# Kernel optimization log

Measured on AMD Instinct MI355X. Metric: run time of the kernel, lower is better.

## Reference

```python
import jax, jax.numpy as jnp
import numpy as np

R = 8
TOP_K_A = 2
TOP_K_B = 2
SCALING = 16.0 / R  # lora_alpha / r


def setup_inputs() -> dict:
    key = jax.random.key(0)
    k1, k2, k3, k4, k5 = jax.random.split(key, 5)
    B, S, D_IN, D_OUT, EA, EB = 4, 2048, 4096, 4096, 8, 8
    x = jax.random.normal(k1, (B, S, D_IN), dtype=jnp.float32)
    router_logits_a = jax.random.normal(k2, (B * S, EA), dtype=jnp.float32)
    router_logits_b = jax.random.normal(k3, (B * S, EB), dtype=jnp.float32)
    # nn.Linear(in, r).weight -> [r, in]; stacked per expert: [E_a, r, in]
    Wa = jax.random.normal(k4, (EA, R, D_IN), dtype=jnp.float32) * (1.0 / np.sqrt(D_IN))
    # nn.Linear(r, out).weight -> [out, r]; stacked: [E_b, out, r]
    Wb = jax.random.normal(k5, (EB, D_OUT, R), dtype=jnp.float32) * (1.0 / np.sqrt(R))
    return {"x": x, "router_logits_a": router_logits_a,
            "router_logits_b": router_logits_b, "Wa": Wa, "Wb": Wb}


def reference(x, router_logits_a, router_logits_b, Wa, Wb):
    B, S, D_IN = x.shape
    flat_x = x.reshape(-1, D_IN)  # [T, D_in]

    # --- A experts: dense compute over all experts, then top-k gather ---
    topk_logits_a, topk_idx_a = jax.lax.top_k(router_logits_a, TOP_K_A)
    weights_a = jax.nn.softmax(topk_logits_a, axis=-1)  # [T, k_a]
    a_all = jnp.einsum('ti,eri->ter', flat_x, Wa)  # [T, E_a, r]
    sel_a = jnp.take_along_axis(a_all, topk_idx_a[:, :, None], axis=1)  # [T, k_a, r]
    mid = jnp.sum(sel_a * weights_a[:, :, None], axis=1)  # [T, r]

    # --- B experts: dense compute over all experts, then top-k gather ---
    b_all = jnp.einsum('tr,eor->teo', mid, Wb)  # [T, E_b, D_out]
    topk_logits_b, topk_idx_b = jax.lax.top_k(router_logits_b, TOP_K_B)
    weights_b = jax.nn.softmax(topk_logits_b, axis=-1)  # [T, k_b]
    sel_b = jnp.take_along_axis(b_all, topk_idx_b[:, :, None], axis=1)  # [T, k_b, D_out]
    out_flat = jnp.sum(sel_b * weights_b[:, :, None], axis=1) * SCALING  # [T, D_out]
    output = out_flat.reshape(B, S, -1)

    # --- load-balancing aux losses (torch.var is unbiased) ---
    probs_a = jnp.mean(jax.nn.softmax(router_logits_a, axis=-1), axis=0)
    probs_b = jnp.mean(jax.nn.softmax(router_logits_b, axis=-1), axis=0)
    aux_loss_a = Wa.shape[0] * jnp.var(probs_a, ddof=1)
    aux_loss_b = Wb.shape[0] * jnp.var(probs_b, ddof=1)
    return output, aux_loss_a, aux_loss_b
```

## Files before the change

kernel.cpp:

```cpp
#include <hip/hip_runtime.h>

#define T_TOK 8192
#define D_IN  4096
#define D_OUT 4096

typedef _Float16 h2 __attribute__((ext_vector_type(2)));
typedef _Float16 h4 __attribute__((ext_vector_type(4)));
typedef _Float16 h8 __attribute__((ext_vector_type(8)));
typedef float    f4v __attribute__((ext_vector_type(4)));

__device__ __forceinline__ h2 pkrtz(float a, float b) {
    auto r = __builtin_amdgcn_cvt_pkrtz(a, b);
    h2 o; __builtin_memcpy(&o, &r, 4); return o;
}
__device__ __forceinline__ h8 cvt8(float4 f0, float4 f1) {
    h2 p0 = pkrtz(f0.x, f0.y), p1 = pkrtz(f0.z, f0.w);
    h2 p2 = pkrtz(f1.x, f1.y), p3 = pkrtz(f1.z, f1.w);
    return (h8){p0.x, p0.y, p1.x, p1.y, p2.x, p2.y, p3.x, p3.y};
}

__device__ __forceinline__ void gl_lds16(const void* g, void* l) {
    __builtin_amdgcn_global_load_lds(
        (const __attribute__((address_space(1))) unsigned int*)g,
        (__attribute__((address_space(3))) unsigned int*)l, 16, 0, 0);
}


__global__ __launch_bounds__(256)
void prep(const float* __restrict__ Wa, const float* __restrict__ Wb,
          const float* __restrict__ la, const float* __restrict__ lb,
          _Float16* __restrict__ WaB, _Float16* __restrict__ WbB,
          double* __restrict__ pax) {
    const int bid = blockIdx.x, tx = threadIdx.x;
    __shared__ double red[4][16];
    if (bid < 256) {
        int gid = bid * 256 + tx;
        int er = gid >> 10, k0 = (gid & 1023) * 4;
        float4 v = ((const float4*)Wa)[gid];
        h2 p0 = pkrtz(v.x, v.y), p1 = pkrtz(v.z, v.w);
        h4 o = { p0.x, p0.y, p1.x, p1.y };
        *(h4*)(WaB + ((k0 >> 3) * 64 + er) * 8 + (k0 & 7)) = o;
    } else if (bid < 384) {
        int gid = (bid - 256) * 256 + tx;
        int e = gid >> 12, o = gid & 4095;
        const float4* p = (const float4*)(Wb + ((size_t)e * 4096 + o) * 8);
        h8 v = cvt8(p[0], p[1]);
        *(h8*)(WbB + ((size_t)e * 4096 + o) * 8) = v;
    } else {
        const int ab = bid - 384;
        const int t = ab * 256 + tx;
        double loc[16];
        {
            float l[8];
#pragma unroll
            for (int i = 0; i < 8; ++i) l[i] = la[(size_t)t * 8 + i];
            float m = l[0];
#pragma unroll
            for (int i = 1; i < 8; ++i) m = fmaxf(m, l[i]);
            float s = 0.f, e[8];
#pragma unroll
            for (int i = 0; i < 8; ++i) { e[i] = __expf(l[i] - m); s += e[i]; }
#pragma unroll
            for (int i = 0; i < 8; ++i) loc[i] = (double)(e[i] / s);
        }
        {
            float l[8];
#pragma unroll
            for (int i = 0; i < 8; ++i) l[i] = lb[(size_t)t * 8 + i];
            float m = l[0];
#pragma unroll
            for (int i = 1; i < 8; ++i) m = fmaxf(m, l[i]);
            float s = 0.f, e[8];
#pragma unroll
            for (int i = 0; i < 8; ++i) { e[i] = __expf(l[i] - m); s += e[i]; }
#pragma unroll
            for (int i = 0; i < 8; ++i) loc[8 + i] = (double)(e[i] / s);
        }
        const int lane = tx & 63, wid = tx >> 6;
#pragma unroll
        for (int v = 0; v < 16; ++v) {
            double s = loc[v];
#pragma unroll
            for (int off = 32; off > 0; off >>= 1) s += __shfl_down(s, off, 64);
            if (lane == 0) red[wid][v] = s;
        }
        __syncthreads();
        if (tx < 16)
            pax[ab * 16 + tx] = red[0][tx] + red[1][tx] + red[2][tx] + red[3][tx];
    }
}

__global__ __launch_bounds__(256)
void fused(const float* __restrict__ x, const _Float16* __restrict__ WaB,
           const _Float16* __restrict__ WbB, const float* __restrict__ la,
           const float* __restrict__ lb, float* __restrict__ out,
           const double* __restrict__ pax) {
    __shared__ union {
        struct { float xb[2][2048]; _Float16 wab[2][8192]; } p1;
        struct { _Float16 wbb[2][8192]; } p3;
    } U;
    __shared__ float    pL[16][66];
    __shared__ _Float16 MbL[1024];
    __shared__ float    sW0[16], sW1[16], sCb[16][8];
    __shared__ int      sE0[16], sE1[16];
    __shared__ double   sl[16];

    const int tx = threadIdx.x, l = tx & 63, w = tx >> 6;
    const int mr = l & 15, kf = l >> 4;
    const int m0 = blockIdx.x * 16;
    const int er1 = w * 16 + mr;

    f4v acc = (f4v){0.f, 0.f, 0.f, 0.f};

#define STAGE1(IT, BUF) do {                                                   \
    _Pragma("unroll") for (int i_ = 0; i_ < 2; ++i_) {                         \
        int j_ = w * 2 + i_;                                                   \
        int row_ = j_ * 2 + (l >> 5);                                          \
        int cb_ = ((l & 31) * 16) ^ ((row_ & 7) << 4);                         \
        const char* src_ = (const char*)x                                      \
            + (((size_t)(m0 + row_) * D_IN + (size_t)(IT) * 128) << 2) + cb_;  \
        gl_lds16(src_, (char*)U.p1.xb[BUF] + j_ * 1024);                       \
    }                                                                          \
    _Pragma("unroll") for (int i_ = 0; i_ < 4; ++i_) {                         \
        int j_ = w * 4 + i_;                                                   \
        const char* src_ = (const char*)WaB + (size_t)(IT) * 16384             \
            + j_ * 1024 + l * 16;                                              \
        gl_lds16(src_, (char*)U.p1.wab[BUF] + j_ * 1024);                      \
    }                                                                          \
  } while (0)

#define CMP1(BUF) do {                                                         \
    const char* xb_ = (const char*)U.p1.xb[BUF] + mr * 512;                    \
    const int sw_ = (mr & 7) << 4;                                             \
    _Pragma("unroll") for (int ks_ = 0; ks_ < 4; ++ks_) {                      \
        int c0_ = ks_ * 128 + kf * 32;                                         \
        float4 f0_ = *(const float4*)(xb_ + ((c0_) ^ sw_));                    \
        float4 f1_ = *(const float4*)(xb_ + ((c0_ + 16) ^ sw_));               \
        h8 a_ = cvt8(f0_, f1_);                                                \
        h8 b_ = *(const h8*)((const char*)U.p1.wab[BUF]                        \
                             + ((ks_ * 4 + kf) * 64 + er1) * 16);              \
        acc = __builtin_amdgcn_mfma_f32_16x16x32_f16(a_, b_, acc, 0, 0, 0);    \
    }                                                                          \
  } while (0)

    STAGE1(0, 0);
    __syncthreads();
#pragma unroll 1
    for (int it = 0; it < 32; ++it) {
        if (it < 31) STAGE1(it + 1, (it & 1) ^ 1);
        CMP1(it & 1);
        __syncthreads();
    }
#undef STAGE1
#undef CMP1

#pragma unroll
    for (int r = 0; r < 4; ++r) pL[kf * 4 + r][er1] = acc[r];
    __syncthreads();

    if (tx < 16) {
        const int t = tx;
        float lg[8];
#pragma unroll
        for (int i = 0; i < 8; ++i) lg[i] = la[(size_t)(m0 + t) * 8 + i];
        int e0 = 0; float b0 = lg[0];
#pragma unroll
        for (int i = 1; i < 8; ++i) if (lg[i] > b0) { b0 = lg[i]; e0 = i; }
        int e1 = -1; float b1 = -1e30f;
#pragma unroll
        for (int i = 0; i < 8; ++i) if (i != e0 && lg[i] > b1) { b1 = lg[i]; e1 = i; }
        float w1 = __expf(b1 - b0), s = 1.f + w1;
        sW0[t] = 1.f / s; sW1[t] = w1 / s; sE0[t] = e0; sE1[t] = e1;

#pragma unroll
        for (int i = 0; i < 8; ++i) lg[i] = lb[(size_t)(m0 + t) * 8 + i];
        int f0 = 0; float c0 = lg[0];
#pragma unroll
        for (int i = 1; i < 8; ++i) if (lg[i] > c0) { c0 = lg[i]; f0 = i; }
        int f1 = -1; float c1 = -1e30f;
#pragma unroll
        for (int i = 0; i < 8; ++i) if (i != f0 && lg[i] > c1) { c1 = lg[i]; f1 = i; }
        float wb1 = __expf(c1 - c0), sb = 1.f + wb1;
        float wb0s = 2.f / sb, wb1s = 2.f * wb1 / sb;
#pragma unroll
        for (int e = 0; e < 8; ++e)
            sCb[t][e] = (e == f0) ? wb0s : (e == f1) ? wb1s : 0.f;
    }
    __syncthreads();

    {
        const int t = tx >> 4, gg = tx & 15;
        const float w0 = sW0[t], w1 = sW1[t];
        const int e0 = sE0[t], e1 = sE1[t];
        const float cb = sCb[t][gg >> 1];
        h4 o;
#pragma unroll
        for (int j = 0; j < 4; ++j) {
            int r = (gg * 4 + j) & 7;
            float mid = w0 * pL[t][e0 * 8 + r] + w1 * pL[t][e1 * 8 + r];
            o[j] = (_Float16)(cb * mid);
        }
        *(h4*)(MbL + ((gg >> 1) * 16 + t) * 8 + (gg & 1) * 4) = o;
    }
    __syncthreads();

    h8 a30 = *(const h8*)(MbL + ((0 * 4 + kf) * 16 + mr) * 8);
    h8 a31 = *(const h8*)(MbL + ((1 * 4 + kf) * 16 + mr) * 8);
    float* outp = out + (size_t)(m0 + kf * 4) * D_OUT;

#define STAGE3(CH, BUF) do {                                                   \
    _Pragma("unroll") for (int i_ = 0; i_ < 4; ++i_) {                         \
        int j_ = w * 4 + i_;                                                   \
        const char* src_ = (const char*)WbB + (size_t)(j_ >> 1) * 65536        \
            + (size_t)(CH) * 2048 + (j_ & 1) * 1024 + l * 16;                  \
        gl_lds16(src_, (char*)U.p3.wbb[BUF] + j_ * 1024);                      \
    }                                                                          \
  } while (0)

#define CMP3(BUF, CH) do {                                                     \
    f4v o0 = (f4v){0.f,0.f,0.f,0.f}, o1 = (f4v){0.f,0.f,0.f,0.f};              \
    _Pragma("unroll") for (int ks_ = 0; ks_ < 2; ++ks_) {                      \
        const char* bb_ = (const char*)U.p3.wbb[BUF]                           \
            + ((ks_ * 4 + kf) * 128 + w * 32 + mr) * 16;                       \
        h8 b0_ = *(const h8*)(bb_);                                            \
        h8 b1_ = *(const h8*)(bb_ + 256);                                      \
        h8 af_ = ks_ ? a31 : a30;                                              \
        o0 = __builtin_amdgcn_mfma_f32_16x16x32_f16(af_, b0_, o0, 0, 0, 0);    \
        o1 = __builtin_amdgcn_mfma_f32_16x16x32_f16(af_, b1_, o1, 0, 0, 0);    \
    }                                                                          \
    int n0_ = (CH) * 128 + w * 32 + mr;                                        \
    _Pragma("unroll") for (int r_ = 0; r_ < 4; ++r_) {                         \
        outp[(size_t)r_ * D_OUT + n0_]      = o0[r_];                          \
        outp[(size_t)r_ * D_OUT + n0_ + 16] = o1[r_]; }                        \
  } while (0)

    STAGE3(0, 0);
    __syncthreads();
#pragma unroll 1
    for (int c = 0; c < 32; ++c) {
        if (c < 31) STAGE3(c + 1, (c & 1) ^ 1);
        CMP3(c & 1, c);
        __syncthreads();
    }
#undef STAGE3
#undef CMP3

    if (blockIdx.x == 0) {
        if (tx < 16) {
            double s = 0.0;
#pragma unroll
            for (int b = 0; b < 32; ++b) s += pax[b * 16 + tx];
            sl[tx] = s;
        }
        __syncthreads();
        if (tx == 0) {
            double pa[8], pb[8], ma = 0.0, mb = 0.0;
            for (int e = 0; e < 8; ++e) { pa[e] = sl[e] / 8192.0;     ma += pa[e] / 8.0; }
            for (int e = 0; e < 8; ++e) { pb[e] = sl[8 + e] / 8192.0; mb += pb[e] / 8.0; }
            double va = 0.0, vb = 0.0;
            for (int e = 0; e < 8; ++e) { double d = pa[e] - ma; va += d * d; }
            for (int e = 0; e < 8; ++e) { double d = pb[e] - mb; vb += d * d; }
            out[(size_t)T_TOK * D_OUT + 0] = (float)(8.0 * va / 7.0);
            out[(size_t)T_TOK * D_OUT + 1] = (float)(8.0 * vb / 7.0);
        }
    }
}

extern "C" void kernel_launch(void* const* d_in, const int* in_sizes, int n_in,
                              void* d_out, int out_size, void* d_ws, size_t ws_size,
                              hipStream_t stream) {
    const float* x  = (const float*)d_in[0];
    const float* la = (const float*)d_in[1];
    const float* lb = (const float*)d_in[2];
    const float* Wa = (const float*)d_in[3];
    const float* Wb = (const float*)d_in[4];
    float* out = (float*)d_out;

    char* ws = (char*)d_ws;
    _Float16* WaB = (_Float16*)ws;
    _Float16* WbB = (_Float16*)(ws + 524288);
    double*   pax = (double*)(ws + 1048576);

    prep<<<416, 256, 0, stream>>>(Wa, Wb, la, lb, WaB, WbB, pax);
    fused<<<512, 256, 0, stream>>>(x, WaB, WbB, la, lb, out, pax);
}
```

Baseline: 269.3 us.

## Use 512-thread blocks with split-K stage one and pre-swizzled weight layouts

Result: slower. 278.2 us (+3.3%).

```diff
diff --git a/kernel.cpp b/kernel.cpp
--- a/kernel.cpp
+++ b/kernel.cpp
@@ -39,13 +39,18 @@
         float4 v = ((const float4*)Wa)[gid];
         h2 p0 = pkrtz(v.x, v.y), p1 = pkrtz(v.z, v.w);
         h4 o = { p0.x, p0.y, p1.x, p1.y };
-        *(h4*)(WaB + ((k0 >> 3) * 64 + er) * 8 + (k0 & 7)) = o;
+        int it = k0 >> 7, ks = (k0 >> 5) & 3, kf = (k0 >> 3) & 3;
+        int g = er >> 4, mr = er & 15;
+        *(h4*)(WaB + it * 8192 + (ks * 4 + g) * 512 + (kf * 16 + mr) * 8
+               + (k0 & 7)) = o;
     } else if (bid < 384) {
         int gid = (bid - 256) * 256 + tx;
         int e = gid >> 12, o = gid & 4095;
         const float4* p = (const float4*)(Wb + ((size_t)e * 4096 + o) * 8);
         h8 v = cvt8(p[0], p[1]);
-        *(h8*)(WbB + ((size_t)e * 4096 + o) * 8) = v;
+        int ch = o >> 7, wv = (o >> 4) & 7, mr = o & 15;
+        *(h8*)(WbB + (size_t)ch * 8192 + ((e >> 2) * 8 + wv) * 512
+               + ((e & 3) * 16 + mr) * 8) = v;
     } else {
         const int ab = bid - 384;
         const int t = ab * 256 + tx;
@@ -90,55 +95,51 @@
     }
 }
 
-__global__ __launch_bounds__(256)
+__global__ __launch_bounds__(512, 4)
 void fused(const float* __restrict__ x, const _Float16* __restrict__ WaB,
            const _Float16* __restrict__ WbB, const float* __restrict__ la,
            const float* __restrict__ lb, float* __restrict__ out,
            const double* __restrict__ pax) {
-    __shared__ union {
-        struct { float xb[2][2048]; _Float16 wab[2][8192]; } p1;
-        struct { _Float16 wbb[2][8192]; } p3;
-    } U;
-    __shared__ float    pL[16][66];
-    __shared__ _Float16 MbL[1024];
-    __shared__ float    sW0[16], sW1[16], sCb[16][8];
-    __shared__ int      sE0[16], sE1[16];
-    __shared__ double   sl[16];
+    __shared__ char S[49152];
+    __shared__ float sW0[16], sW1[16], sCb[16][8];
+    __shared__ int   sE0[16], sE1[16];
+    __shared__ double sl[16];
 
     const int tx = threadIdx.x, l = tx & 63, w = tx >> 6;
     const int mr = l & 15, kf = l >> 4;
     const int m0 = blockIdx.x * 16;
-    const int er1 = w * 16 + mr;
+    const int g  = w & 3;
+    const int kh = w >> 2;
+    const int er1 = g * 16 + mr;
+    float* pLp = (float*)(S + 32768);
+    _Float16* MbLp = (_Float16*)(S + 41216);
 
     f4v acc = (f4v){0.f, 0.f, 0.f, 0.f};
 
 #define STAGE1(IT, BUF) do {                                                   \
+    _Pragma("unroll") for (int i_ = 0; i_ < 3; ++i_) {                         \
+        int p_ = w * 3 + i_;                                                   \
+        if (p_ < 8) {                                                          \
+            const char* src_ = (const char*)x + (size_t)(m0 + mr) * 16384      \
+                + (size_t)(IT) * 512 + (p_ >> 1) * 128 + kf * 32 + (p_ & 1) * 16; \
+            gl_lds16(src_, S + (BUF) * 8192 + p_ * 1024);                      \
+        } else {                                                               \
+            int q_ = p_ - 8;                                                   \
+            const char* src_ = (const char*)WaB + (size_t)(IT) * 16384         \
+                + q_ * 1024 + l * 16;                                          \
+            gl_lds16(src_, S + 16384 + (BUF) * 16384 + q_ * 1024);             \
+        }                                                                      \
+    }                                                                          \
+  } while (0)
+
+#define CMP1(BUF) do {                                                         \
     _Pragma("unroll") for (int i_ = 0; i_ < 2; ++i_) {                         \
-        int j_ = w * 2 + i_;                                                   \
-        int row_ = j_ * 2 + (l >> 5);                                          \
-        int cb_ = ((l & 31) * 16) ^ ((row_ & 7) << 4);                         \
-        const char* src_ = (const char*)x                                      \
-            + (((size_t)(m0 + row_) * D_IN + (size_t)(IT) * 128) << 2) + cb_;  \
-        gl_lds16(src_, (char*)U.p1.xb[BUF] + j_ * 1024);                       \
-    }                                                                          \
-    _Pragma("unroll") for (int i_ = 0; i_ < 4; ++i_) {                         \
-        int j_ = w * 4 + i_;                                                   \
-        const char* src_ = (const char*)WaB + (size_t)(IT) * 16384             \
-            + j_ * 1024 + l * 16;                                              \
-        gl_lds16(src_, (char*)U.p1.wab[BUF] + j_ * 1024);                      \
-    }                                                                          \
-  } while (0)
-
-#define CMP1(BUF) do {                                                         \
-    const char* xb_ = (const char*)U.p1.xb[BUF] + mr * 512;                    \
-    const int sw_ = (mr & 7) << 4;                                             \
-    _Pragma("unroll") for (int ks_ = 0; ks_ < 4; ++ks_) {                      \
-        int c0_ = ks_ * 128 + kf * 32;                                         \
-        float4 f0_ = *(const float4*)(xb_ + ((c0_) ^ sw_));                    \
-        float4 f1_ = *(const float4*)(xb_ + ((c0_ + 16) ^ sw_));               \
+        int ks_ = kh * 2 + i_;                                                 \
+        float4 f0_ = *(const float4*)(S + (BUF) * 8192 + (ks_ * 2) * 1024 + l * 16);     \
+        float4 f1_ = *(const float4*)(S + (BUF) * 8192 + (ks_ * 2 + 1) * 1024 + l * 16); \
         h8 a_ = cvt8(f0_, f1_);                                                \
-        h8 b_ = *(const h8*)((const char*)U.p1.wab[BUF]                        \
-                             + ((ks_ * 4 + kf) * 64 + er1) * 16);              \
+        h8 b_ = *(const h8*)(S + 16384 + (BUF) * 16384                         \
+                             + (ks_ * 4 + g) * 1024 + l * 16);                 \
         acc = __builtin_amdgcn_mfma_f32_16x16x32_f16(a_, b_, acc, 0, 0, 0);    \
     }                                                                          \
   } while (0)
@@ -155,7 +156,7 @@
 #undef CMP1
 
 #pragma unroll
-    for (int r = 0; r < 4; ++r) pL[kf * 4 + r][er1] = acc[r];
+    for (int r = 0; r < 4; ++r) pLp[kh * 1056 + (kf * 4 + r) * 66 + er1] = acc[r];
     __syncthreads();
 
     if (tx < 16) {
@@ -188,7 +189,7 @@
     }
     __syncthreads();
 
-    {
+    if (tx < 256) {
         const int t = tx >> 4, gg = tx & 15;
         const float w0 = sW0[t], w1 = sW1[t];
         const int e0 = sE0[t], e1 = sE1[t];
@@ -197,41 +198,36 @@
 #pragma unroll
         for (int j = 0; j < 4; ++j) {
             int r = (gg * 4 + j) & 7;
-            float mid = w0 * pL[t][e0 * 8 + r] + w1 * pL[t][e1 * 8 + r];
+            float mid = w0 * (pLp[t * 66 + e0 * 8 + r] + pLp[1056 + t * 66 + e0 * 8 + r])
+                      + w1 * (pLp[t * 66 + e1 * 8 + r] + pLp[1056 + t * 66 + e1 * 8 + r]);
             o[j] = (_Float16)(cb * mid);
         }
-        *(h4*)(MbL + ((gg >> 1) * 16 + t) * 8 + (gg & 1) * 4) = o;
-    }
-    __syncthreads();
-
-    h8 a30 = *(const h8*)(MbL + ((0 * 4 + kf) * 16 + mr) * 8);
-    h8 a31 = *(const h8*)(MbL + ((1 * 4 + kf) * 16 + mr) * 8);
+        *(h4*)(MbLp + ((gg >> 1) * 16 + t) * 8 + (gg & 1) * 4) = o;
+    }
+    __syncthreads();
+
+    h8 a30 = *(const h8*)(MbLp + ((0 * 4 + kf) * 16 + mr) * 8);
+    h8 a31 = *(const h8*)(MbLp + ((1 * 4 + kf) * 16 + mr) * 8);
     float* outp = out + (size_t)(m0 + kf * 4) * D_OUT;
 
 #define STAGE3(CH, BUF) do {                                                   \
-    _Pragma("unroll") for (int i_ = 0; i_ < 4; ++i_) {                         \
-        int j_ = w * 4 + i_;                                                   \
-        const char* src_ = (const char*)WbB + (size_t)(j_ >> 1) * 65536        \
-            + (size_t)(CH) * 2048 + (j_ & 1) * 1024 + l * 16;                  \
-        gl_lds16(src_, (char*)U.p3.wbb[BUF] + j_ * 1024);                      \
+    _Pragma("unroll") for (int i_ = 0; i_ < 2; ++i_) {                         \
+        int p_ = w * 2 + i_;                                                   \
+        const char* src_ = (const char*)WbB + (size_t)(CH) * 16384             \
+            + p_ * 1024 + l * 16;                                              \
+        gl_lds16(src_, S + (BUF) * 16384 + p_ * 1024);                         \
     }                                                                          \
   } while (0)
 
 #define CMP3(BUF, CH) do {                                                     \
-    f4v o0 = (f4v){0.f,0.f,0.f,0.f}, o1 = (f4v){0.f,0.f,0.f,0.f};              \
-    _Pragma("unroll") for (int ks_ = 0; ks_ < 2; ++ks_) {                      \
-        const char* bb_ = (const char*)U.p3.wbb[BUF]                           \
-            + ((ks_ * 4 + kf) * 128 + w * 32 + mr) * 16;                       \
-        h8 b0_ = *(const h8*)(bb_);                                            \
-        h8 b1_ = *(const h8*)(bb_ + 256);                                      \
-        h8 af_ = ks_ ? a31 : a30;                                              \
-        o0 = __builtin_amdgcn_mfma_f32_16x16x32_f16(af_, b0_, o0, 0, 0, 0);    \
-        o1 = __builtin_amdgcn_mfma_f32_16x16x32_f16(af_, b1_, o1, 0, 0, 0);    \
-    }                                                                          \
-    int n0_ = (CH) * 128 + w * 32 + mr;                                        \
-    _Pragma("unroll") for (int r_ = 0; r_ < 4; ++r_) {                         \
-        outp[(size_t)r_ * D_OUT + n0_]      = o0[r_];                          \
-        outp[(size_t)r_ * D_OUT + n0_ + 16] = o1[r_]; }                        \
+    f4v o0 = (f4v){0.f,0.f,0.f,0.f};                                           \
+    h8 b0_ = *(const h8*)(S + (BUF) * 16384 + (0 * 8 + w) * 1024 + l * 16);    \
+    h8 b1_ = *(const h8*)(S + (BUF) * 16384 + (1 * 8 + w) * 1024 + l * 16);    \
+    o0 = __builtin_amdgcn_mfma_f32_16x16x32_f16(a30, b0_, o0, 0, 0, 0);        \
+    o0 = __builtin_amdgcn_mfma_f32_16x16x32_f16(a31, b1_, o0, 0, 0, 0);        \
+    int n0_ = (CH) * 128 + w * 16 + mr;                                        \
+    _Pragma("unroll") for (int r_ = 0; r_ < 4; ++r_)                           \
+        outp[(size_t)r_ * D_OUT + n0_] = o0[r_];                               \
   } while (0)
 
     STAGE3(0, 0);
@@ -282,5 +278,5 @@
     double*   pax = (double*)(ws + 1048576);
 
     prep<<<416, 256, 0, stream>>>(Wa, Wb, la, lb, WaB, WbB, pax);
-    fused<<<512, 256, 0, stream>>>(x, WaB, WbB, la, lb, out, pax);
-}
+    fused<<<512, 512, 0, stream>>>(x, WaB, WbB, la, lb, out, pax);
+}
```
